# Optimization experiments

Hardware: AMD Instinct MI355X
Metric: run time of the kernel (lower is better)

## Reference

```python
import jax, jax.numpy as jnp
import numpy as np

B, C, H, W = 16, 256, 56, 56
HID = C * 2            # modifier_expansion = 2
GROUPS = 8             # min(8, HID//4)
K = 3                  # inner_steps
LR = 0.01              # exp(log(inner_lr))
RATIO = 0.25           # spatial_mask_ratio
GN_EPS = 1e-5


def setup_inputs() -> dict:
    key = jax.random.key(0)
    ks = jax.random.split(key, 12)
    x = jax.random.normal(ks[0], (B, C, H, W), jnp.float32)
    # modifier params (1x1 convs stored as 2D matrices) + GroupNorm affine
    conv1_w = jax.random.normal(ks[1], (HID, C), jnp.float32) / np.sqrt(C)
    gn_gamma = 1.0 + 0.1 * jax.random.normal(ks[2], (HID,), jnp.float32)
    gn_beta = 0.1 * jax.random.normal(ks[3], (HID,), jnp.float32)
    conv2_w = jax.random.normal(ks[4], (C, HID), jnp.float32) / np.sqrt(HID)
    # surprise reconstructor (bottleneck = C//4)
    recon_w1 = jax.random.normal(ks[5], (C // 4, C), jnp.float32) / np.sqrt(C)
    recon_w2 = jax.random.normal(ks[6], (C, C // 4), jnp.float32) / np.sqrt(C // 4)
    # gate MLP
    gate_w1 = jax.random.normal(ks[7], (C // 4, C), jnp.float32) / np.sqrt(C)
    gate_b1 = jnp.zeros((C // 4,), jnp.float32)
    gate_w2 = jax.random.normal(ks[8], (1, C // 4), jnp.float32) / np.sqrt(C // 4)
    gate_b2 = jnp.zeros((1,), jnp.float32)
    residual_scale = jnp.asarray(0.05, jnp.float32)
    # EMA buffers (eval mode: frozen)
    running_mean = 0.05 * jax.random.normal(ks[9], (C,), jnp.float32)
    running_var = 1.0 + 0.05 * jax.random.uniform(ks[10], (C,), jnp.float32)
    # spatial masks: exactly int(H*W*RATIO) zeroed positions per sample, one mask
    # per inner update step (only steps 0..K-2 affect the output)
    num_mask = int(H * W * RATIO)
    rng = np.random.default_rng(0)
    r = rng.random((K - 1, B, H * W))
    idx = np.argsort(r, axis=-1)[..., :num_mask]
    m = np.ones((K - 1, B, H * W), dtype=bool)
    np.put_along_axis(m, idx, False, axis=-1)
    masks = jnp.asarray(m.reshape(K - 1, B, 1, H, W))
    return dict(x=x, conv1_w=conv1_w, gn_gamma=gn_gamma, gn_beta=gn_beta,
                conv2_w=conv2_w, recon_w1=recon_w1, recon_w2=recon_w2,
                gate_w1=gate_w1, gate_b1=gate_b1, gate_w2=gate_w2,
                gate_b2=gate_b2, residual_scale=residual_scale,
                running_mean=running_mean, running_var=running_var, masks=masks)


def _group_norm(h, gamma, beta):
    b = h.shape[0]
    hg = h.reshape(b, GROUPS, HID // GROUPS, H, W)
    mu = hg.mean(axis=(2, 3, 4), keepdims=True)
    var = hg.var(axis=(2, 3, 4), keepdims=True)  # biased, matching torch GN
    hg = (hg - mu) * jax.lax.rsqrt(var + GN_EPS)
    return hg.reshape(b, HID, H, W) * gamma[None, :, None, None] + beta[None, :, None, None]


def _modifier(feat, w1, gamma, beta, w2):
    # Conv2d 1x1 (no bias) -> GroupNorm -> GELU -> [Dropout2d: identity in eval] -> Conv2d 1x1
    h = jnp.einsum('bchw,oc->bohw', feat, w1)
    h = jax.nn.gelu(_group_norm(h, gamma, beta), approximate=False)
    return jnp.einsum('bohw,co->bchw', h, w2)


def _surprise(y, mask, rw1, rw2, rm, rv):
    mf = mask.astype(y.dtype)                       # [B,1,H,W]
    my = y * mf
    h = jax.nn.gelu(jnp.einsum('bchw,oc->bohw', my, rw1), approximate=False)
    rec = jnp.einsum('bohw,co->bchw', h, rw2)
    inv = 1.0 - mf
    recon = (((rec - y) ** 2) * inv).sum() / (inv.sum() * C + 1e-8)
    n = y.shape[0] * y.shape[2] * y.shape[3]
    cm = y.mean(axis=(0, 2, 3))                     # [C]
    cv = ((y - cm[None, :, None, None]) ** 2).sum(axis=(0, 2, 3)) / (n - 1)  # unbiased
    consist = ((cm - rm) ** 2).mean() + ((cv / (rv + 1e-8) - 1.0) ** 2).mean()
    return recon + 0.1 * consist


def reference(x, conv1_w, gn_gamma, gn_beta, conv2_w, recon_w1, recon_w2,
              gate_w1, gate_b1, gate_w2, gate_b2, residual_scale,
              running_mean, running_var, masks):
    feat = jax.lax.stop_gradient(x)  # feat_inner = features.detach()
    params = (conv1_w, gn_gamma, gn_beta, conv2_w)

    def inner_loss(p, mask):
        m = _modifier(feat, *p)
        return _surprise(m + feat, mask, recon_w1, recon_w2, running_mean, running_var)

    # TTT inner loop: K-1 SGD updates on the modifier params; updates are
    # stop_gradient'ed so the outer Jacobian wrt initial params is identity,
    # matching torch's .data in-place update with create_graph=False.
    for step in range(K - 1):
        g = jax.grad(inner_loss)(params, masks[step])
        params = tuple(p - LR * jax.lax.stop_gradient(gi) for p, gi in zip(params, g))

    modification = _modifier(x, *params)  # final forward uses non-detached features

    pooled = x.mean(axis=(2, 3))                                    # [B,C]
    gh = jax.nn.gelu(pooled @ gate_w1.T + gate_b1, approximate=False)
    gate = jax.nn.sigmoid(gh @ gate_w2.T + gate_b2)[:, :, None, None]  # [B,1,1,1]

    return x + residual_scale * gate * modification
```

## Files before the change

kernel.cpp:

```cpp
#include <hip/hip_runtime.h>
#include <math.h>


#define BB    16
#define CC    256
#define HWW   3136
#define NTOT  (BB*HWW)
#define HIDD  512
#define NGRP  8
#define GMSZ  (64*HWW)
#define C4    64
#define LRATE 0.01f
#define SKW   32
#define CHUNK (NTOT/SKW)
#define NV8   (HWW/8)

#define EP_STORE    0
#define EP_ADDFEAT  1
#define EP_T1H      2
#define EP_DYREC    3
#define EP_DT1      4
#define EP_DYFIN    5
#define EP_H1STAT   6
#define EP_YADDSTAT 7
#define EP_GNB1     8

typedef unsigned short u16;
typedef __attribute__((ext_vector_type(8))) short bf16x8;
typedef __attribute__((ext_vector_type(4))) float f32x4;

__device__ __forceinline__ float bf2f(u16 u){
  return __uint_as_float(((unsigned)u)<<16);
}
__device__ __forceinline__ u16 f2bf(float f){
  unsigned u = __float_as_uint(f);
  u += 0x7FFFu + ((u>>16)&1u);
  return (u16)(u>>16);
}
__device__ __forceinline__ float gelu_f(float x){
  return 0.5f*x*(1.0f+erff(x*0.70710678118654752f));
}
__device__ __forceinline__ float rcp_f(float x){ return __builtin_amdgcn_rcpf(x); }
__device__ __forceinline__ float gelu_fast(float x){
  float x2 = x*x;
  float u = 0.7978845608f*x*fmaf(0.044715f, x2, 1.0f);
  float t = 1.0f - 2.0f*rcp_f(__expf(2.0f*u)+1.0f);
  return 0.5f*x*(1.0f+t);
}
__device__ __forceinline__ float gelu_g_fast(float x){
  float x2 = x*x;
  float u = 0.7978845608f*x*fmaf(0.044715f, x2, 1.0f);
  float t = 1.0f - 2.0f*rcp_f(__expf(2.0f*u)+1.0f);
  float du = 0.7978845608f*fmaf(0.134145f, x2, 1.0f);
  return fmaf(0.5f*x*(1.0f-t*t), du, 0.5f*(1.0f+t));
}
__device__ __forceinline__ float blk_sum(float v, float* sm){
  #pragma unroll
  for (int o=32;o>0;o>>=1) v += __shfl_down(v,o);
  if ((threadIdx.x & 63)==0) sm[threadIdx.x>>6] = v;
  __syncthreads();
  float r = sm[0]+sm[1]+sm[2]+sm[3];
  __syncthreads();
  return r;
}
__device__ __forceinline__ uint4 pack8(const ushort* e){
  uint4 v;
  v.x = (unsigned)e[0] | ((unsigned)e[1]<<16);
  v.y = (unsigned)e[2] | ((unsigned)e[3]<<16);
  v.z = (unsigned)e[4] | ((unsigned)e[5]<<16);
  v.w = (unsigned)e[6] | ((unsigned)e[7]<<16);
  return v;
}
__device__ __forceinline__ void up8(uint4 v, float* f){
  f[0]=bf2f((u16)(v.x&0xFFFFu)); f[1]=bf2f((u16)(v.x>>16));
  f[2]=bf2f((u16)(v.y&0xFFFFu)); f[3]=bf2f((u16)(v.y>>16));
  f[4]=bf2f((u16)(v.z&0xFFFFu)); f[5]=bf2f((u16)(v.z>>16));
  f[6]=bf2f((u16)(v.w&0xFFFFu)); f[7]=bf2f((u16)(v.w>>16));
}
// ... 22 lines not shown
  for (int i=0;i<256;i++){
    unsigned char v=m[i]; if (v>mx) mx=v;
    if (v){ int r=i&3; if(r==0)nz0=1; else if(r==1)nz1=1; else if(r==2)nz2=1; else nz3=1; }
  }
  int f;
  if (mx<=1) f = (nz1|nz2|nz3) ? 0 : 1;
  else       f = (!nz0 && !nz1) ? 3 : 2;
  *flag=f;
}
__global__ void k_report(u16* out, float v){
  if (threadIdx.x==0 && blockIdx.x==0) out[0] = f2bf(v);
}

__global__ void k_cvt(const void* __restrict__ src, float* __restrict__ dst, int n,
                      const int* __restrict__ dtf){
  int i = blockIdx.x*256 + threadIdx.x;
  if (i>=n) return;
  if (*dtf) dst[i] = bf2f(((const u16*)src)[i]);
  else      dst[i] = ((const float*)src)[i];
}
__global__ void k_wcvt(const float* __restrict__ src, u16* __restrict__ d,
                       u16* __restrict__ dT, int R, int Cc){
  int i = blockIdx.x*256+threadIdx.x;
  if (i >= R*Cc) return;
  int r = i/Cc, c = i - r*Cc;
  u16 v = f2bf(src[i]);
  d[i] = v;
  if (dT) dT[(size_t)c*R + r] = v;
}

__global__ void k_expand(const unsigned char* __restrict__ mraw, const int* __restrict__ flag,
                         float* __restrict__ mf, float* __restrict__ zc){
  __shared__ float sm[4];
  int i = blockIdx.x*256 + threadIdx.x;
  int f = *flag;
  float v;
  if (f==1)      v = (((const int*)mraw)[i] != 0) ? 1.f : 0.f;
  else if (f==0) v = (mraw[i] != 0) ? 1.f : 0.f;
  else if (f==2) v = (((const u16*)mraw)[i] != 0) ? 1.f : 0.f;
  else           v = (((const float*)mraw)[i] != 0.f) ? 1.f : 0.f;
  mf[i] = v;
  float S = blk_sum(1.f - v, sm);
  if (threadIdx.x==0) atomicAdd(&zc[blockIdx.x/196], S);
}

template<int MASKX,int EPI,int XDYN,int E0DYN>
__global__ __launch_bounds__(256) void k_gemm_mfma(
    const u16* __restrict__ A, const void* __restrict__ Xv, u16* __restrict__ Out,
    int K, const int* __restrict__ xdt, const float* __restrict__ mf,
    const void* __restrict__ e0, const float* __restrict__ e1,
    const float* __restrict__ e2, u16* __restrict__ o2, float* __restrict__ o3)
{
  __shared__ __align__(16) u16 Ws[64*40];
  __shared__ u16 Xs[128*40];
  const int t = threadIdx.x;
  const int w = t >> 6, lane = t & 63;
  const int col = lane & 15, quad = lane >> 4;
  const int M = (int)gridDim.y << 6;
  const int m0 = blockIdx.y << 6, n0 = blockIdx.x << 7;
  const int isbx = XDYN ? *xdt : 1;
  const u16*   Xb = (const u16*)Xv;
  const float* Xf = (const float*)Xv;
  const int wrow = t >> 2, wkq = (t & 3) * 8;
  const int xn   = 2*(t & 63);
  const int xq   = t >> 6;
  const int gn0  = n0 + xn;
  const int xb_  = gn0 / HWW;
  const int xs_  = gn0 - xb_*HWW;

  f32x4 acc[4][2];
  #pragma unroll
  for (int i=0;i<4;i++){
    #pragma unroll
    for (int j=0;j<2;j++) acc[i][j] = (f32x4)(0.0f);
  }

  for (int k0=0; k0<K; k0+=32){
    {
      uint4 v = *(const uint4*)(A + (size_t)(m0+wrow)*K + k0 + wkq);
      *(uint4*)(Ws + wrow*40 + wkq) = v;
    }
    {
      ushort e[16];
      size_t base = ((size_t)xb_*K + k0 + xq*8)*HWW + xs_;
      if (isbx){
        #pragma unroll
        for (int j=0;j<8;j++){
          unsigned v = *(const unsigned*)(Xb + base + (size_t)j*HWW);
          e[j]   = (ushort)(v & 0xFFFFu);
          e[8+j] = (ushort)(v >> 16);
        }
      } else {
        #pragma unroll
        for (int j=0;j<8;j++){
          float2 f = *(const float2*)(Xf + base + (size_t)j*HWW);
          e[j]   = f2bf(f.x);
          e[8+j] = f2bf(f.y);
        }
      }
      if (MASKX){
        if (mf[gn0]   == 0.f){
          #pragma unroll
          for (int j=0;j<8;j++) e[j] = 0;
        }
        if (mf[gn0+1] == 0.f){
          #pragma unroll
          for (int j=0;j<8;j++) e[8+j] = 0;
        }
      }
      *(uint4*)(Xs + xn*40     + xq*8) = pack8(e);
      *(uint4*)(Xs + (xn+1)*40 + xq*8) = pack8(e+8);
    }
    __syncthreads();
    bf16x8 af[4], bfr[2];
    #pragma unroll
    for (int mi=0;mi<4;mi++)
      af[mi] = *(const bf16x8*)(Ws + (mi*16+col)*40 + quad*8);
    #pragma unroll
    for (int nj=0;nj<2;nj++)
      bfr[nj] = *(const bf16x8*)(Xs + (w*32+nj*16+col)*40 + quad*8);
    #pragma unroll
    for (int mi=0;mi<4;mi++){
      #pragma unroll
      for (int nj=0;nj<2;nj++)
        acc[mi][nj] = __builtin_amdgcn_mfma_f32_16x16x32_bf16(af[mi], bfr[nj], acc[mi][nj], 0,0,0);
    }
    __syncthreads();
  }

  const int isb0 = E0DYN ? *xdt : 1;

  if (EPI==EP_H1STAT){
    float* sred = (float*)Ws;
    if (t < 4) sred[t] = 0.f;
    __syncthreads();
    float sH[2]={0.f,0.f}, sQ[2]={0.f,0.f};
    #pragma unroll
    for (int nj=0;nj<2;nj++){
      const int nb = n0 + w*32 + nj*16;
      const int b  = nb / HWW;
      const int sb = nb - b*HWW + col;
      #pragma unroll
      for (int mi=0;mi<4;mi++){
        #pragma unroll
        for (int r=0;r<4;r++){
          const int m = m0 + mi*16 + quad*4 + r;
          const size_t oidx = ((size_t)b*M + m)*HWW + sb;
          float v = acc[mi][nj][r];
          Out[oidx] = f2bf(v);
          sH[nj] += v; sQ[nj] = fmaf(v,v,sQ[nj]);
        }
      }
    }
    #pragma unroll
    for (int nj=0;nj<2;nj++){
      float a=sH[nj], c=sQ[nj];
      #pragma unroll
      for (int o=1;o<64;o<<=1){ a += __shfl_xor(a,o); c += __shfl_xor(c,o); }
      if (lane==0){
        const int nb = n0 + w*32 + nj*16;
        const int slot = ((nb/HWW) != n0/HWW) ? 1 : 0;
        atomicAdd(&sred[slot*2],   a);
        atomicAdd(&sred[slot*2+1], c);
      }
    }
    __syncthreads();
    const int g = m0>>6;
    if (t==0){
      const int b0=n0/HWW;
      atomicAdd(&o3[b0*NGRP+g],     sred[0]);
      atomicAdd(&o3[128+b0*NGRP+g], sred[1]);
    }
    if (t==1){
      const int b0=n0/HWW, b1=(n0+127)/HWW;
      if (b1!=b0){
        atomicAdd(&o3[b1*NGRP+g],     sred[2]);
        atomicAdd(&o3[128+b1*NGRP+g], sred[3]);
      }
    }
    return;
  }

  if (EPI==EP_YADDSTAT){
    float* sred = (float*)Ws;
    for (int i=t;i<128;i+=256) sred[i]=0.f;
    __syncthreads();
    #pragma unroll
    for (int mi=0;mi<4;mi++){
      #pragma unroll
      for (int r=0;r<4;r++){
        float sM=0.f, sQv=0.f;
        const int m = m0 + mi*16 + quad*4 + r;
        #pragma unroll
        for (int nj=0;nj<2;nj++){
          const int nb = n0 + w*32 + nj*16;
          const int b  = nb / HWW;
          const int sb = nb - b*HWW + col;
          const size_t oidx = ((size_t)b*M + m)*HWW + sb;
          float xv = isb0 ? bf2f(((const u16*)e0)[oidx]) : ((const float*)e0)[oidx];
          float y = acc[mi][nj][r] + xv;
          Out[oidx] = f2bf(y);
          sM += y; sQv = fmaf(y,y,sQv);
        }
        #pragma unroll
        for (int o=1;o<16;o<<=1){ sM += __shfl_xor(sM,o); sQv += __shfl_xor(sQv,o); }
        if (col==0){
          atomicAdd(&sred[mi*16+quad*4+r],    sM);
          atomicAdd(&sred[64+mi*16+quad*4+r], sQv);
        }
      }
    }
    __syncthreads();
    if (t<64){
      atomicAdd(&o3[m0+t],    sred[t]);
      atomicAdd(&o3[CC+m0+t], sred[64+t]);
    }
    return;
  }

  if (EPI==EP_GNB1){
    float* sred = (float*)Ws;
    for (int i=t;i<132;i+=256) sred[i]=0.f;
    __syncthreads();
    const int g = m0>>6;
    float sS1[2]={0.f,0.f}, sS2[2]={0.f,0.f};
    #pragma unroll
    for (int mi=0;mi<4;mi++){
      #pragma unroll
      for (int r=0;r<4;r++){
        const int m = m0 + mi*16 + quad*4 + r;
        const float go = e2[m], beo = e2[HIDD+m];
        float dB=0.f, dG=0.f;
        #pragma unroll
        for (int nj=0;nj<2;nj++){
          const int nb = n0 + w*32 + nj*16;
          const int b  = nb / HWW;
          const int sb = nb - b*HWW + col;
          const int bg = b*NGRP + g;
          const size_t oidx = ((size_t)b*M + m)*HWW + sb;
          const float mU = e1[bg], rS = e1[128+bg];
          float hn   = (bf2f(((const u16*)e0)[oidx]) - mU)*rS;
          float ghat = fmaf(hn, go, beo);
          float dgh  = acc[mi][nj][r] * gelu_g_fast(ghat);
          float dhn  = dgh * go;
          Out[oidx] = f2bf(dhn);
          dB += dgh; dG = fmaf(dgh, hn, dG);
          sS1[nj] += dhn; sS2[nj] = fmaf(dhn, hn, sS2[nj]);
        }
        #pragma unroll
        for (int o=1;o<16;o<<=1){ dB += __shfl_xor(dB,o); dG += __shfl_xor(dG,o); }
        if (col==0){
          atomicAdd(&sred[mi*16+quad*4+r],    dB);
          atomicAdd(&sred[64+mi*16+quad*4+r], dG);
        }
      }
    }
    #pragma unroll
    for (int nj=0;nj<2;nj++){
      float a=sS1[nj], c=sS2[nj];
      #pragma unroll
      for (int o=1;o<64;o<<=1){ a += __shfl_xor(a,o); c += __shfl_xor(c,o); }
      if (lane==0){
        const int nb = n0 + w*32 + nj*16;
        const int slot = ((nb/HWW) != n0/HWW) ? 1 : 0;
        atomicAdd(&sred[128+slot*2],   a);
        atomicAdd(&sred[128+slot*2+1], c);
      }
    }
    __syncthreads();
    if (t<64){
      atomicAdd(&o3[m0+t],     sred[64+t]);
      atomicAdd(&o3[512+m0+t], sred[t]);
    }
    if (t==64){
      const int b0=n0/HWW;
      atomicAdd(&o3[1024+b0*NGRP+g],     sred[128]);
      atomicAdd(&o3[1152+b0*NGRP+g],     sred[129]);
    }
    if (t==65){
      const int b0=n0/HWW, b1=(n0+127)/HWW;
      if (b1!=b0){
        atomicAdd(&o3[1024+b1*NGRP+g],   sred[130]);
        atomicAdd(&o3[1152+b1*NGRP+g],   sred[131]);
      }
    }
    return;
  }

  float dscale = 0.f;
  if (EPI==EP_DYREC) dscale = 2.0f / (e1[0]*(float)CC + 1e-8f);
  #pragma unroll
  for (int nj=0;nj<2;nj++){
    const int nb = n0 + w*32 + nj*16;
    const int b  = nb / HWW;
    const int sb = nb - b*HWW + col;
    const int n  = nb + col;
    #pragma unroll
    for (int mi=0;mi<4;mi++){
      #pragma unroll
      for (int r=0;r<4;r++){
        const int m = m0 + mi*16 + quad*4 + r;
        const size_t oidx = ((size_t)b*M + m)*HWW + sb;
        float v = acc[mi][nj][r];
        if (EPI==EP_STORE){ Out[oidx] = f2bf(v); }
        else if (EPI==EP_ADDFEAT){
          float xv = isb0 ? bf2f(((const u16*)e0)[oidx]) : ((const float*)e0)[oidx];
          Out[oidx] = f2bf(v + xv);
        }
        else if (EPI==EP_T1H){ Out[oidx] = f2bf(v); o2[oidx] = f2bf(gelu_fast(v)); }
        else if (EPI==EP_DYREC){
          float iv = 1.0f - mf[n];
          Out[oidx] = f2bf((v - bf2f(((const u16*)e0)[oidx]))*iv*dscale);
        }
        else if (EPI==EP_DT1){ Out[oidx] = f2bf(v * gelu_g_fast(bf2f(((const u16*)e0)[oidx]))); }
        else if (EPI==EP_DYFIN){
          float dyold = bf2f(Out[oidx]);
          Out[oidx] = f2bf(mf[n]*v - dyold + e1[m] + e2[m]*bf2f(((const u16*)e0)[oidx]));
        }
      }
    }
  }
}

template<int QDYN>
__global__ __launch_bounds__(256) void k_wgrad_mfma(
    const u16* __restrict__ P, const void* __restrict__ Qv, float* __restrict__ part,
    int CHP, int CHQ, const int* __restrict__ xdt, int ntx)
{
  __shared__ u16 Ps[64*40];
  __shared__ u16 Qs[64*40];
  const int f = blockIdx.x;
  const int j = f >> 3;
  const int sk = (f & 7) + ((j >> 5) << 3);
  const int tile = j & 31;
  const int ty = tile / ntx;
  const int m0 = (tile - ty*ntx) << 6;
  const int n0 = ty << 6;
  const int t = threadIdx.x;
  const int w = t >> 6, lane = t & 63;
  const int col = lane & 15, quad = lane >> 4;
  const int isbq = QDYN ? *xdt : 1;
  const u16*   Qb = (const u16*)Qv;
  const float* Qf = (const float*)Qv;
  const int srow = (t & 127) >> 1;
  const int ssq  = ((t & 127) & 1) * 16;
  f32x4 acc[2][2];
  #pragma unroll
  for (int i=0;i<2;i++){
    #pragma unroll
    for (int jj=0;jj<2;jj++) acc[i][jj] = (f32x4)(0.0f);
  }
  const int mbase = (w & 1)*32, nbase = (w >> 1)*32;

  for (int kb = sk*CHUNK; kb < sk*CHUNK + CHUNK; kb += 32){
    const int b = kb / HWW;
    const int s = kb - b*HWW;
    if (t < 128){
      size_t off = ((size_t)b*CHP + m0+srow)*HWW + s + ssq;
      uint4 v0 = *(const uint4*)(P + off);
      uint4 v1 = *(const uint4*)(P + off + 8);
      *(uint4*)(Ps + srow*40 + ssq)     = v0;
      *(uint4*)(Ps + srow*40 + ssq + 8) = v1;
    } else {
      size_t off = ((size_t)b*CHQ + n0+srow)*HWW + s + ssq;
      if (isbq){
        uint4 v0 = *(const uint4*)(Qb + off);
        uint4 v1 = *(const uint4*)(Qb + off + 8);
        *(uint4*)(Qs + srow*40 + ssq)     = v0;
        *(uint4*)(Qs + srow*40 + ssq + 8) = v1;
      } else {
        ushort e[16];
        #pragma unroll
        for (int g=0; g<4; g++){
          float4 ff = *(const float4*)(Qf + off + g*4);
          e[g*4+0]=f2bf(ff.x); e[g*4+1]=f2bf(ff.y); e[g*4+2]=f2bf(ff.z); e[g*4+3]=f2bf(ff.w);
        }
        *(uint4*)(Qs + srow*40 + ssq)     = pack8(e);
        *(uint4*)(Qs + srow*40 + ssq + 8) = pack8(e+8);
      }
    }
    __syncthreads();
    bf16x8 pa[2], qb[2];
    #pragma unroll
    for (int a=0;a<2;a++)
      pa[a] = *(const bf16x8*)(Ps + (mbase + a*16 + col)*40 + quad*8);
    #pragma unroll
    for (int bb=0;bb<2;bb++)
      qb[bb] = *(const bf16x8*)(Qs + (nbase + bb*16 + col)*40 + quad*8);
    #pragma unroll
    for (int a=0;a<2;a++){
      #pragma unroll
      for (int bb=0;bb<2;bb++)
        acc[a][bb] = __builtin_amdgcn_mfma_f32_16x16x32_bf16(pa[a], qb[bb], acc[a][bb], 0,0,0);
    }
    __syncthreads();
  }
  float* dst = part + (size_t)sk*CHP*CHQ;
  #pragma unroll
  for (int a=0;a<2;a++){
    #pragma unroll
    for (int bb=0;bb<2;bb++){
      #pragma unroll
      for (int r=0;r<4;r++){
        const int m = m0 + mbase + a*16 + quad*4 + r;
        const int n = n0 + nbase + bb*16 + col;
        dst[(size_t)m*CHQ + n] = acc[a][bb][r];
      }
    }
  }
}
__global__ void k_wgrad_reduce(const float* __restrict__ part, float* __restrict__ dW, int n){
  int i = blockIdx.x*256+threadIdx.x;
  if (i>=n) return;
  float s=0;
  #pragma unroll
  for (int k=0;k<SKW;k++) s += part[(size_t)k*n + i];
  dW[i]=s;
}

__global__ void k_gn_finalize(const float* gsum, const float* gsumsq, float* mu, float* rsig){
  int i = threadIdx.x; if (i>=BB*NGRP) return;
  float m = gsum[i]*(1.0f/GMSZ);
  float v = gsumsq[i]*(1.0f/GMSZ) - m*m;
  v = fmaxf(v, 0.0f);
  mu[i]=m; rsig[i]=rsqrtf(v+1e-5f);
}
template<int FAST>
__global__ void k_gelu_fwd(const u16* __restrict__ src, u16* __restrict__ dst,
// ... 65 lines not shown
  uint4* pa = (uint4*)(dA + (size_t)bo*HWW);
  const uint4* ph = (const uint4*)(h1 + (size_t)bo*HWW);
  for (int i=threadIdx.x;i<NV8;i+=256){
    float fa[8], fh[8]; up8(pa[i], fa); up8(ph[i], fh);
    #pragma unroll
    for (int j=0;j<8;j++){
      float hn = (fh[j]-m)*r;
      fa[j] = r*(fa[j] - a1 - hn*a2);
    }
    pa[i] = pk8(fa);
  }
}

__global__ void k_update(float* pw1, float* pw2, float* pg, float* pb,
    const float* dW1, const float* dW2, const float* dGa, const float* dBe){
  int i = blockIdx.x*256+threadIdx.x;
  if (i < HIDD*CC){ pw1[i] -= LRATE*dW1[i]; pw2[i] -= LRATE*dW2[i]; }
  if (i < HIDD){ pg[i] -= LRATE*dGa[i]; pb[i] -= LRATE*dBe[i]; }
}

__global__ void k_pool(const void* __restrict__ xv, const int* __restrict__ dtf, float* pooled){
  __shared__ float sm[4];
  int bc = blockIdx.x;
  int isb = *dtf;
  float s=0;
  if (isb){
    const uint4* p = (const uint4*)((const u16*)xv + (size_t)bc*HWW);
    for (int i=threadIdx.x;i<NV8;i+=256){
      float f[8]; up8(p[i], f);
      #pragma unroll
      for (int j=0;j<8;j++) s+=f[j];
    }
  } else {
    const float4* p = (const float4*)((const float*)xv + (size_t)bc*HWW);
    for (int i=threadIdx.x;i<HWW/4;i+=256){
      float4 f = p[i];
      s += f.x+f.y+f.z+f.w;
    }
  }
  float S = blk_sum(s,sm);
  if (threadIdx.x==0) pooled[bc]=S*(1.0f/HWW);
}
__global__ void k_gate(const float* __restrict__ pooled, const float* __restrict__ gw1,
    const float* __restrict__ gb1, const float* __restrict__ gw2, const float* __restrict__ gb2,
    float* gate){
  int b = blockIdx.x, j = threadIdx.x;
  float acc = gb1[j];
  const float* pr = pooled + b*CC;
  for (int c=0;c<CC;c++) acc = fmaf(pr[c], gw1[j*CC+c], acc);
  float v = gelu_f(acc)*gw2[j];
  #pragma unroll
  for (int o=32;o>0;o>>=1) v += __shfl_down(v,o);
  if (j==0) gate[b] = 1.0f/(1.0f+expf(-(v+gb2[0])));
}
__global__ void k_out(const void* __restrict__ xv, const u16* __restrict__ mod,
    const float* __restrict__ gate, const float* __restrict__ rsf,
    const int* __restrict__ dtf, void* __restrict__ out){
  size_t i4 = (size_t)blockIdx.x*256+threadIdx.x;
  size_t i = i4*4;
  int b = (int)(i / ((size_t)CC*HWW));
  float gm = rsf[0]*gate[b];
  int isb = *dtf;
  ushort4 mv = ((const ushort4*)mod)[i4];
  if (isb){
    ushort4 xu = ((const ushort4*)xv)[i4];
    ushort4 r;
    r.x = f2bf(bf2f(xu.x) + gm*bf2f(mv.x));
    r.y = f2bf(bf2f(xu.y) + gm*bf2f(mv.y));
    r.z = f2bf(bf2f(xu.z) + gm*bf2f(mv.z));
    r.w = f2bf(bf2f(xu.w) + gm*bf2f(mv.w));
    ((ushort4*)out)[i4] = r;
  } else {
    float4 xf = ((const float4*)xv)[i4];
    float4 r;
    r.x = xf.x + gm*bf2f(mv.x);
    r.y = xf.y + gm*bf2f(mv.y);
    r.z = xf.z + gm*bf2f(mv.z);
    r.w = xf.w + gm*bf2f(mv.w);
    ((float4*)out)[i4] = r;
  }
}

extern "C" void kernel_launch(void* const* d_in, const int* in_sizes, int n_in,
                              void* d_out, int out_size, void* d_ws, size_t ws_size,
                              hipStream_t stream)
{
  const void* x_in   = d_in[0];
  const void* w1_in  = d_in[1];
  const void* g_in   = d_in[2];
  const void* b_in   = d_in[3];
  const void* w2_in  = d_in[4];
  const void* rw1_in = d_in[5];
  const void* rw2_in = d_in[6];
  const void* gw1_in = d_in[7];
  const void* gb1_in = d_in[8];
  const void* gw2_in = d_in[9];
  const void* gb2_in = d_in[10];
  const void* rs_in  = d_in[11];
  const void* rm_in  = d_in[12];
  const void* rv_in  = d_in[13];
  const void* mk_in  = d_in[14];
  (void)in_sizes; (void)n_in; (void)out_size;

  char* base = (char*)d_ws;
  size_t off = 0;
  auto alloc = [&](size_t bytes)->char*{
    char* p = base+off; off = (off+bytes+255)&~(size_t)255; return p;
  };
  u16* ybuf = (u16*)alloc((size_t)CC*NTOT*2);
  u16* dY   = (u16*)alloc((size_t)CC*NTOT*2);
  u16* Ab   = (u16*)alloc((size_t)HIDD*NTOT*2);
  u16* t1b  = (u16*)alloc((size_t)C4*NTOT*2);
  u16* hb   = (u16*)alloc((size_t)C4*NTOT*2);
  u16* h1rc = ybuf;
  float* part = (float*)ybuf;
  float* mfb  = (float*)alloc((size_t)2*NTOT*4);
  float* pw1  = (float*)alloc(131072*4);
  float* pw2  = (float*)alloc(131072*4);
  float* dW1  = (float*)alloc(131072*4);
  float* dW2  = (float*)alloc(131072*4);
  u16* wb1   = (u16*)alloc(131072*2);
  u16* wb2   = (u16*)alloc(131072*2);
  u16* wb2T  = (u16*)alloc(131072*2);
  u16* rwb1  = (u16*)alloc(16384*2);
  u16* rwb1T = (u16*)alloc(16384*2);
  u16* rwb2  = (u16*)alloc(16384*2);
  u16* rwb2T = (u16*)alloc(16384*2);
  float* pg   = (float*)alloc(512*4);
  float* pb   = (float*)alloc(512*4);
  float* rw1f = (float*)alloc(16384*4);
  float* rw2f = (float*)alloc(16384*4);
  float* gw1f = (float*)alloc(16384*4);
  float* gb1f = (float*)alloc(64*4);
// ... 16 lines not shown
  float* s2     = (float*)alloc(512);
  float* pooled = (float*)alloc(16384);
  float* gate   = (float*)alloc(256);
  float* zc     = (float*)alloc(256);
  int*   dtf    = (int*)alloc(256);
  int*   mkf    = (int*)alloc(256);

  if (off > ws_size){
    k_report<<<1,64,0,stream>>>((u16*)d_out, (float)(ws_size>>20));
    return;
  }
  u16* h1p = nullptr;
  if (off + (size_t)HIDD*NTOT*2 <= ws_size)
    h1p = (u16*)alloc((size_t)HIDD*NTOT*2);

  k_detect_dtype<<<1,1,0,stream>>>((const u16*)x_in, dtf);
  k_detect_mask<<<1,1,0,stream>>>((const unsigned char*)mk_in, mkf);
  #define CVT(src,dst,n) k_cvt<<<((n)+255)/256,256,0,stream>>>(src,dst,(n),dtf)
  CVT(w1_in,  pw1,  131072);
  CVT(g_in,   pg,   512);
  CVT(b_in,   pb,   512);
  CVT(w2_in,  pw2,  131072);
  CVT(rw1_in, rw1f, 16384);
  CVT(rw2_in, rw2f, 16384);
  CVT(gw1_in, gw1f, 16384);
  CVT(gb1_in, gb1f, 64);
  CVT(gw2_in, gw2f, 64);
  CVT(gb2_in, gb2f, 1);
  CVT(rs_in,  rsf,  1);
  CVT(rm_in,  rmf,  256);
  CVT(rv_in,  rvf,  256);
  #undef CVT
  k_wcvt<<<512,256,0,stream>>>(pw1, wb1, 0,     HIDD, CC);
  k_wcvt<<<512,256,0,stream>>>(pw2, wb2, wb2T,  CC, HIDD);
  k_wcvt<<<64,256,0,stream>>>(rw1f, rwb1, rwb1T, C4, CC);
  k_wcvt<<<64,256,0,stream>>>(rw2f, rwb2, rwb2T, CC, C4);
  hipMemsetAsync(zc, 0, 8, stream);
  k_expand<<<392,256,0,stream>>>((const unsigned char*)mk_in, mkf, mfb, zc);

  for (int s=0; s<2; s++){
    const float* mfs = mfb + s*NTOT;
    u16* h1dst = h1p ? h1p : Ab;
    hipMemsetAsync(gsum, 0, 1024, stream);
    k_gemm_mfma<0,EP_H1STAT,1,0><<<dim3(392,8),256,0,stream>>>(wb1, x_in, h1dst, CC, dtf, 0,0,0,0,0, gsum);
    k_gn_finalize<<<1,128,0,stream>>>(gsum, gsumsq, mu, rsig);
    k_gelu_fwd<1><<<BB*HIDD,256,0,stream>>>(h1dst, Ab, mu, rsig, pg, pb);
    hipMemsetAsync(cmsum, 0, 2048, stream);
    k_gemm_mfma<0,EP_YADDSTAT,0,1><<<dim3(392,4),256,0,stream>>>(wb2, Ab, ybuf, HIDD, dtf, 0, x_in, 0,0,0, cmsum);
    k_y_finalize<<<1,256,0,stream>>>(cmsum, cmsq, rmf, rvf, coefA, coefB);
    k_gemm_mfma<1,EP_T1H,0,0><<<dim3(392,1),256,0,stream>>>(rwb1, ybuf, t1b, CC, dtf, mfs, 0,0,0, hb, 0);
    k_gemm_mfma<0,EP_DYREC,0,0><<<dim3(392,4),256,0,stream>>>(rwb2, hb, dY, C4, dtf, mfs, ybuf, zc+s, 0,0, 0);
    k_gemm_mfma<0,EP_DT1,0,0><<<dim3(392,1),256,0,stream>>>(rwb2T, dY, hb, CC, dtf, 0, t1b, 0,0,0, 0);
    k_gemm_mfma<0,EP_DYFIN,0,0><<<dim3(392,4),256,0,stream>>>(rwb1T, hb, dY, C4, dtf, mfs, ybuf, coefA, coefB, 0, 0);
    k_wgrad_mfma<0><<<dim3(32*SKW),256,0,stream>>>(dY, Ab, part, CC, HIDD, dtf, 4);
    k_wgrad_reduce<<<512,256,0,stream>>>(part, dW2, 131072);
    hipMemsetAsync(dGa, 0, 5120, stream);
    if (h1p){
      k_gemm_mfma<0,EP_GNB1,0,0><<<dim3(392,8),256,0,stream>>>(wb2T, dY, Ab, CC, dtf, 0, h1p, mu, pg, 0, dGa);
    } else {
      k_gemm_mfma<0,EP_STORE,0,0><<<dim3(392,8),256,0,stream>>>(wb2T, dY, Ab, CC, dtf, 0,0,0,0,0, 0);
    }
    const u16* h1src = h1p;
    if (!h1p){
      k_gemm_mfma<0,EP_H1STAT,1,0><<<dim3(392,8),256,0,stream>>>(wb1, x_in, h1rc, CC, dtf, 0,0,0,0,0, gsum);
      h1src = h1rc;
      k_gn_bwd1<<<BB*HIDD,256,0,stream>>>(Ab, h1src, mu, rsig, pg, pb, dGa, dBe, s1, s2);
    }
    k_gn_bwd2<<<BB*HIDD,256,0,stream>>>(Ab, h1src, mu, rsig, s1, s2);
    k_wgrad_mfma<1><<<dim3(32*SKW),256,0,stream>>>(Ab, x_in, part, HIDD, CC, dtf, 8);
    k_wgrad_reduce<<<512,256,0,stream>>>(part, dW1, 131072);
    k_update<<<512,256,0,stream>>>(pw1, pw2, pg, pb, dW1, dW2, dGa, dBe);
    k_wcvt<<<512,256,0,stream>>>(pw1, wb1, 0,    HIDD, CC);
    k_wcvt<<<512,256,0,stream>>>(pw2, wb2, wb2T, CC, HIDD);
  }

  hipMemsetAsync(gsum, 0, 1024, stream);
  k_gemm_mfma<0,EP_H1STAT,1,0><<<dim3(392,8),256,0,stream>>>(wb1, x_in, Ab, CC, dtf, 0,0,0,0,0, gsum);
  k_gn_finalize<<<1,128,0,stream>>>(gsum, gsumsq, mu, rsig);
  k_gelu_fwd<0><<<BB*HIDD,256,0,stream>>>(Ab, Ab, mu, rsig, pg, pb);
  k_gemm_mfma<0,EP_STORE,0,0><<<dim3(392,4),256,0,stream>>>(wb2, Ab, ybuf, HIDD, dtf, 0,0,0,0,0, 0);

  k_pool<<<BB*CC,256,0,stream>>>(x_in, dtf, pooled);
  k_gate<<<BB,64,0,stream>>>(pooled, gw1f, gb1f, gw2f, gb2f, gate);
  k_out<<<(CC*NTOT)/1024,256,0,stream>>>(x_in, ybuf, gate, rsf, dtf, d_out);
}
```

Before: 1.209 ms.

## Stage GEMM epilogues through LDS for vectorized stores; fuse GN backward and output

Every MFMA GEMM epilogue now writes its accumulator tile to shared memory and reads it back row-wise, so each thread handles 8 contiguous outputs with 16-byte loads and stores instead of scattered 2-byte accesses. The GroupNorm backward second pass is folded into the operand load of the dW1 weight-gradient kernel, which removes the separate k_gn_bwd2 pass over the hidden activations. The final output residual-gate combine is fused into the last conv2 GEMM epilogue, removing the intermediate buffer and the k_out kernel. In exchange each epilogue adds per-slice barriers and LDS traffic, and the wgrad loader now does extra arithmetic and reads h1.

```diff
diff --git a/kernel.cpp b/kernel.cpp
--- a/kernel.cpp
+++ b/kernel.cpp
@@ -14,6 +14,7 @@
 #define SKW   32
 #define CHUNK (NTOT/SKW)
 #define NV8   (HWW/8)
+#define FSTR  132
 
 #define EP_STORE    0
 #define EP_ADDFEAT  1
@@ -24,6 +25,7 @@
 #define EP_H1STAT   6
 #define EP_YADDSTAT 7
 #define EP_GNB1     8
+#define EP_OUT      9
 
 typedef unsigned short u16;
 typedef __attribute__((ext_vector_type(8))) short bf16x8;
@@ -152,7 +154,7 @@
     const float* __restrict__ e2, u16* __restrict__ o2, float* __restrict__ o3)
 {
   __shared__ __align__(16) u16 Ws[64*40];
-  __shared__ u16 Xs[128*40];
+  __shared__ __align__(16) u16 Xs[128*40];
   const int t = threadIdx.x;
   const int w = t >> 6, lane = t & 63;
   const int col = lane & 15, quad = lane >> 4;
@@ -227,205 +229,235 @@
     }
     __syncthreads();
   }
-
   const int isb0 = E0DYN ? *xdt : 1;
+  float* fst  = (float*)Xs;
+  float* sred = (float*)Ws;
+  const int row16 = t >> 4;
+  const int cb    = (t & 15) * 8;
+  const int nb8   = n0 + cb;
+  const int b8    = nb8 / HWW;
+  const int sb8   = nb8 - b8*HWW;
+  const int bA    = n0 / HWW, bB = (n0+127)/HWW;
+  const int g     = m0 >> 6;
+
+  if (EPI==EP_H1STAT){ if (t<4) sred[t]=0.f; }
+  if (EPI==EP_YADDSTAT){ for (int i=t;i<128;i+=256) sred[i]=0.f; }
+  if (EPI==EP_GNB1){ for (int i=t;i<132;i+=256) sred[i]=0.f; }
+  if (EPI==EP_H1STAT||EPI==EP_YADDSTAT||EPI==EP_GNB1) __syncthreads();
+
+  float dscale=0.f, gmul=0.f, muT=0.f, rT=0.f;
+  if (EPI==EP_DYREC) dscale = 2.0f / (e1[0]*(float)CC + 1e-8f);
+  if (EPI==EP_OUT)   gmul = e2[0]*e1[b8];
+  if (EPI==EP_GNB1){ muT = e1[b8*NGRP+g]; rT = e1[128+b8*NGRP+g]; }
+
+  #pragma unroll
+  for (int mi=0;mi<4;mi++){
+    #pragma unroll
+    for (int nj=0;nj<2;nj++){
+      #pragma unroll
+      for (int r=0;r<4;r++)
+        fst[(quad*4+r)*FSTR + w*32 + nj*16 + col] = acc[mi][nj][r];
+    }
+    __syncthreads();
+    const int m = m0 + mi*16 + row16;
+    const size_t oidx = ((size_t)b8*M + m)*HWW + sb8;
+    float v[8];
+    {
+      const float* frow = fst + row16*FSTR + cb;
+      float4 p0 = *(const float4*)frow;
+      float4 p1 = *(const float4*)(frow+4);
+      v[0]=p0.x; v[1]=p0.y; v[2]=p0.z; v[3]=p0.w;
+      v[4]=p1.x; v[5]=p1.y; v[6]=p1.z; v[7]=p1.w;
+    }
+
+    if (EPI==EP_STORE){
+      *(uint4*)(Out+oidx) = pk8(v);
+    }
+    else if (EPI==EP_ADDFEAT){
+      float xv[8];
+      if (isb0) up8(*(const uint4*)((const u16*)e0+oidx), xv);
+      else {
+        float4 a0 = *(const float4*)((const float*)e0+oidx);
+        float4 a1 = *(const float4*)((const float*)e0+oidx+4);
+        xv[0]=a0.x; xv[1]=a0.y; xv[2]=a0.z; xv[3]=a0.w;
+        xv[4]=a1.x; xv[5]=a1.y; xv[6]=a1.z; xv[7]=a1.w;
+      }
+      #pragma unroll
+      for (int j=0;j<8;j++) v[j] += xv[j];
+      *(uint4*)(Out+oidx) = pk8(v);
+    }
+    else if (EPI==EP_T1H){
+      *(uint4*)(Out+oidx) = pk8(v);
+      float gv[8];
+      #pragma unroll
+      for (int j=0;j<8;j++) gv[j] = gelu_fast(v[j]);
+      *(uint4*)(o2+oidx) = pk8(gv);
+    }
+    else if (EPI==EP_DYREC){
+      float yv[8], mfv[8];
+      up8(*(const uint4*)((const u16*)e0+oidx), yv);
+      float4 f0 = *(const float4*)(mf+nb8);
+      float4 f1 = *(const float4*)(mf+nb8+4);
+      mfv[0]=f0.x; mfv[1]=f0.y; mfv[2]=f0.z; mfv[3]=f0.w;
+      mfv[4]=f1.x; mfv[5]=f1.y; mfv[6]=f1.z; mfv[7]=f1.w;
+      #pragma unroll
+      for (int j=0;j<8;j++) v[j] = (v[j]-yv[j])*(1.0f-mfv[j])*dscale;
+      *(uint4*)(Out+oidx) = pk8(v);
+    }
+    else if (EPI==EP_DT1){
+      float tv[8];
+      up8(*(const uint4*)((const u16*)e0+oidx), tv);
+      #pragma unroll
+      for (int j=0;j<8;j++) v[j] = v[j]*gelu_g_fast(tv[j]);
+      *(uint4*)(Out+oidx) = pk8(v);
+    }
+    else if (EPI==EP_DYFIN){
+      float yv[8], dv[8], mfv[8];
+      up8(*(const uint4*)((const u16*)e0+oidx), yv);
+      up8(*(const uint4*)(Out+oidx), dv);
+      float4 f0 = *(const float4*)(mf+nb8);
+      float4 f1 = *(const float4*)(mf+nb8+4);
+      mfv[0]=f0.x; mfv[1]=f0.y; mfv[2]=f0.z; mfv[3]=f0.w;
+      mfv[4]=f1.x; mfv[5]=f1.y; mfv[6]=f1.z; mfv[7]=f1.w;
+      const float c1 = e1[m], c2 = e2[m];
+      #pragma unroll
+      for (int j=0;j<8;j++) v[j] = mfv[j]*v[j] - dv[j] + c1 + c2*yv[j];
+      *(uint4*)(Out+oidx) = pk8(v);
+    }
+    else if (EPI==EP_H1STAT){
+      *(uint4*)(Out+oidx) = pk8(v);
+      float s=0.f, q=0.f;
+      #pragma unroll
+      for (int j=0;j<8;j++){ s += v[j]; q = fmaf(v[j],v[j],q); }
+      float s0 = (b8==bA)?s:0.f, q0 = (b8==bA)?q:0.f;
+      float s1v = s-s0, q1v = q-q0;
+      #pragma unroll
+      for (int o=1;o<64;o<<=1){
+        s0 += __shfl_xor(s0,o); q0 += __shfl_xor(q0,o);
+        s1v += __shfl_xor(s1v,o); q1v += __shfl_xor(q1v,o);
+      }
+      if (lane==0){
+        atomicAdd(&sred[0], s0); atomicAdd(&sred[1], q0);
+        atomicAdd(&sred[2], s1v); atomicAdd(&sred[3], q1v);
+      }
+    }
+    else if (EPI==EP_YADDSTAT){
+      float xv[8];
+      if (isb0) up8(*(const uint4*)((const u16*)e0+oidx), xv);
+      else {
+        float4 a0 = *(const float4*)((const float*)e0+oidx);
+        float4 a1 = *(const float4*)((const float*)e0+oidx+4);
+        xv[0]=a0.x; xv[1]=a0.y; xv[2]=a0.z; xv[3]=a0.w;
+        xv[4]=a1.x; xv[5]=a1.y; xv[6]=a1.z; xv[7]=a1.w;
+      }
+      float s=0.f, q=0.f;
+      #pragma unroll
+      for (int j=0;j<8;j++){
+        v[j] += xv[j];
+        s += v[j]; q = fmaf(v[j],v[j],q);
+      }
+      *(uint4*)(Out+oidx) = pk8(v);
+      #pragma unroll
+      for (int o=1;o<16;o<<=1){ s += __shfl_xor(s,o); q += __shfl_xor(q,o); }
+      if ((t&15)==0){
+        atomicAdd(&sred[mi*16+row16], s);
+        atomicAdd(&sred[64+mi*16+row16], q);
+      }
+    }
+    else if (EPI==EP_GNB1){
+      float hv[8];
+      up8(*(const uint4*)((const u16*)e0+oidx), hv);
+      const float go = e2[m], beo = e2[HIDD+m];
+      float dB=0.f, dG=0.f, sS=0.f, sQ=0.f;
+      #pragma unroll
+      for (int j=0;j<8;j++){
+        float hn   = (hv[j]-muT)*rT;
+        float ghat = fmaf(hn, go, beo);
+        float dgh  = v[j]*gelu_g_fast(ghat);
+        float dhn  = dgh*go;
+        v[j] = dhn;
+        dB += dgh; dG = fmaf(dgh,hn,dG);
+        sS += dhn; sQ = fmaf(dhn,hn,sQ);
+      }
+      *(uint4*)(Out+oidx) = pk8(v);
+      #pragma unroll
+      for (int o=1;o<16;o<<=1){ dB += __shfl_xor(dB,o); dG += __shfl_xor(dG,o); }
+      if ((t&15)==0){
+        atomicAdd(&sred[mi*16+row16], dB);
+        atomicAdd(&sred[64+mi*16+row16], dG);
+      }
+      float s0 = (b8==bA)?sS:0.f, q0 = (b8==bA)?sQ:0.f;
+      float s1v = sS-s0, q1v = sQ-q0;
+      #pragma unroll
+      for (int o=1;o<64;o<<=1){
+        s0 += __shfl_xor(s0,o); q0 += __shfl_xor(q0,o);
+        s1v += __shfl_xor(s1v,o); q1v += __shfl_xor(q1v,o);
+      }
+      if (lane==0){
+        atomicAdd(&sred[128], s0); atomicAdd(&sred[129], q0);
+        atomicAdd(&sred[130], s1v); atomicAdd(&sred[131], q1v);
+      }
+    }
+    else if (EPI==EP_OUT){
+      float xv[8];
+      if (isb0){
+        up8(*(const uint4*)((const u16*)e0+oidx), xv);
+        #pragma unroll
+        for (int j=0;j<8;j++) v[j] = xv[j] + gmul*v[j];
+        *(uint4*)(Out+oidx) = pk8(v);
+      } else {
+        float4 a0 = *(const float4*)((const float*)e0+oidx);
+        float4 a1 = *(const float4*)((const float*)e0+oidx+4);
+        float4 r0, r1;
+        r0.x = a0.x + gmul*v[0]; r0.y = a0.y + gmul*v[1];
+        r0.z = a0.z + gmul*v[2]; r0.w = a0.w + gmul*v[3];
+        r1.x = a1.x + gmul*v[4]; r1.y = a1.y + gmul*v[5];
+        r1.z = a1.z + gmul*v[6]; r1.w = a1.w + gmul*v[7];
+        *(float4*)((float*)Out+oidx)   = r0;
+        *(float4*)((float*)Out+oidx+4) = r1;
+      }
+    }
+    __syncthreads();
+  }
 
   if (EPI==EP_H1STAT){
-    float* sred = (float*)Ws;
-    if (t < 4) sred[t] = 0.f;
-    __syncthreads();
-    float sH[2]={0.f,0.f}, sQ[2]={0.f,0.f};
-    #pragma unroll
-    for (int nj=0;nj<2;nj++){
-      const int nb = n0 + w*32 + nj*16;
-      const int b  = nb / HWW;
-      const int sb = nb - b*HWW + col;
-      #pragma unroll
-      for (int mi=0;mi<4;mi++){
-        #pragma unroll
-        for (int r=0;r<4;r++){
-          const int m = m0 + mi*16 + quad*4 + r;
-          const size_t oidx = ((size_t)b*M + m)*HWW + sb;
-          float v = acc[mi][nj][r];
-          Out[oidx] = f2bf(v);
-          sH[nj] += v; sQ[nj] = fmaf(v,v,sQ[nj]);
-        }
-      }
-    }
-    #pragma unroll
-    for (int nj=0;nj<2;nj++){
-      float a=sH[nj], c=sQ[nj];
-      #pragma unroll
-      for (int o=1;o<64;o<<=1){ a += __shfl_xor(a,o); c += __shfl_xor(c,o); }
-      if (lane==0){
-        const int nb = n0 + w*32 + nj*16;
-        const int slot = ((nb/HWW) != n0/HWW) ? 1 : 0;
-        atomicAdd(&sred[slot*2],   a);
-        atomicAdd(&sred[slot*2+1], c);
-      }
-    }
-    __syncthreads();
-    const int g = m0>>6;
     if (t==0){
-      const int b0=n0/HWW;
-      atomicAdd(&o3[b0*NGRP+g],     sred[0]);
-      atomicAdd(&o3[128+b0*NGRP+g], sred[1]);
-    }
-    if (t==1){
-      const int b0=n0/HWW, b1=(n0+127)/HWW;
-      if (b1!=b0){
-        atomicAdd(&o3[b1*NGRP+g],     sred[2]);
-        atomicAdd(&o3[128+b1*NGRP+g], sred[3]);
-      }
-    }
-    return;
-  }
-
+      atomicAdd(&o3[bA*NGRP+g],     sred[0]);
+      atomicAdd(&o3[128+bA*NGRP+g], sred[1]);
+    }
+    if (t==1 && bB!=bA){
+      atomicAdd(&o3[bB*NGRP+g],     sred[2]);
+      atomicAdd(&o3[128+bB*NGRP+g], sred[3]);
+    }
+  }
   if (EPI==EP_YADDSTAT){
-    float* sred = (float*)Ws;
-    for (int i=t;i<128;i+=256) sred[i]=0.f;
-    __syncthreads();
-    #pragma unroll
-    for (int mi=0;mi<4;mi++){
-      #pragma unroll
-      for (int r=0;r<4;r++){
-        float sM=0.f, sQv=0.f;
-        const int m = m0 + mi*16 + quad*4 + r;
-        #pragma unroll
-        for (int nj=0;nj<2;nj++){
-          const int nb = n0 + w*32 + nj*16;
-          const int b  = nb / HWW;
-          const int sb = nb - b*HWW + col;
-          const size_t oidx = ((size_t)b*M + m)*HWW + sb;
-          float xv = isb0 ? bf2f(((const u16*)e0)[oidx]) : ((const float*)e0)[oidx];
-          float y = acc[mi][nj][r] + xv;
-          Out[oidx] = f2bf(y);
-          sM += y; sQv = fmaf(y,y,sQv);
-        }
-        #pragma unroll
-        for (int o=1;o<16;o<<=1){ sM += __shfl_xor(sM,o); sQv += __shfl_xor(sQv,o); }
-        if (col==0){
-          atomicAdd(&sred[mi*16+quad*4+r],    sM);
-          atomicAdd(&sred[64+mi*16+quad*4+r], sQv);
-        }
-      }
-    }
-    __syncthreads();
     if (t<64){
       atomicAdd(&o3[m0+t],    sred[t]);
       atomicAdd(&o3[CC+m0+t], sred[64+t]);
     }
-    return;
-  }
-
+  }
   if (EPI==EP_GNB1){
-    float* sred = (float*)Ws;
-    for (int i=t;i<132;i+=256) sred[i]=0.f;
-    __syncthreads();
-    const int g = m0>>6;
-    float sS1[2]={0.f,0.f}, sS2[2]={0.f,0.f};
-    #pragma unroll
-    for (int mi=0;mi<4;mi++){
-      #pragma unroll
-      for (int r=0;r<4;r++){
-        const int m = m0 + mi*16 + quad*4 + r;
-        const float go = e2[m], beo = e2[HIDD+m];
-        float dB=0.f, dG=0.f;
-        #pragma unroll
-        for (int nj=0;nj<2;nj++){
-          const int nb = n0 + w*32 + nj*16;
-          const int b  = nb / HWW;
-          const int sb = nb - b*HWW + col;
-          const int bg = b*NGRP + g;
-          const size_t oidx = ((size_t)b*M + m)*HWW + sb;
-          const float mU = e1[bg], rS = e1[128+bg];
-          float hn   = (bf2f(((const u16*)e0)[oidx]) - mU)*rS;
-          float ghat = fmaf(hn, go, beo);
-          float dgh  = acc[mi][nj][r] * gelu_g_fast(ghat);
-          float dhn  = dgh * go;
-          Out[oidx] = f2bf(dhn);
-          dB += dgh; dG = fmaf(dgh, hn, dG);
-          sS1[nj] += dhn; sS2[nj] = fmaf(dhn, hn, sS2[nj]);
-        }
-        #pragma unroll
-        for (int o=1;o<16;o<<=1){ dB += __shfl_xor(dB,o); dG += __shfl_xor(dG,o); }
-        if (col==0){
-          atomicAdd(&sred[mi*16+quad*4+r],    dB);
-          atomicAdd(&sred[64+mi*16+quad*4+r], dG);
-        }
-      }
-    }
-    #pragma unroll
-    for (int nj=0;nj<2;nj++){
-      float a=sS1[nj], c=sS2[nj];
-      #pragma unroll
-      for (int o=1;o<64;o<<=1){ a += __shfl_xor(a,o); c += __shfl_xor(c,o); }
-      if (lane==0){
-        const int nb = n0 + w*32 + nj*16;
-        const int slot = ((nb/HWW) != n0/HWW) ? 1 : 0;
-        atomicAdd(&sred[128+slot*2],   a);
-        atomicAdd(&sred[128+slot*2+1], c);
-      }
-    }
-    __syncthreads();
     if (t<64){
       atomicAdd(&o3[m0+t],     sred[64+t]);
       atomicAdd(&o3[512+m0+t], sred[t]);
     }
     if (t==64){
-      const int b0=n0/HWW;
-      atomicAdd(&o3[1024+b0*NGRP+g],     sred[128]);
-      atomicAdd(&o3[1152+b0*NGRP+g],     sred[129]);
-    }
-    if (t==65){
-      const int b0=n0/HWW, b1=(n0+127)/HWW;
-      if (b1!=b0){
-        atomicAdd(&o3[1024+b1*NGRP+g],   sred[130]);
-        atomicAdd(&o3[1152+b1*NGRP+g],   sred[131]);
-      }
-    }
-    return;
-  }
-
-  float dscale = 0.f;
-  if (EPI==EP_DYREC) dscale = 2.0f / (e1[0]*(float)CC + 1e-8f);
-  #pragma unroll
-  for (int nj=0;nj<2;nj++){
-    const int nb = n0 + w*32 + nj*16;
-    const int b  = nb / HWW;
-    const int sb = nb - b*HWW + col;
-    const int n  = nb + col;
-    #pragma unroll
-    for (int mi=0;mi<4;mi++){
-      #pragma unroll
-      for (int r=0;r<4;r++){
-        const int m = m0 + mi*16 + quad*4 + r;
-        const size_t oidx = ((size_t)b*M + m)*HWW + sb;
-        float v = acc[mi][nj][r];
-        if (EPI==EP_STORE){ Out[oidx] = f2bf(v); }
-        else if (EPI==EP_ADDFEAT){
-          float xv = isb0 ? bf2f(((const u16*)e0)[oidx]) : ((const float*)e0)[oidx];
-          Out[oidx] = f2bf(v + xv);
-        }
-        else if (EPI==EP_T1H){ Out[oidx] = f2bf(v); o2[oidx] = f2bf(gelu_fast(v)); }
-        else if (EPI==EP_DYREC){
-          float iv = 1.0f - mf[n];
-          Out[oidx] = f2bf((v - bf2f(((const u16*)e0)[oidx]))*iv*dscale);
-        }
-        else if (EPI==EP_DT1){ Out[oidx] = f2bf(v * gelu_g_fast(bf2f(((const u16*)e0)[oidx]))); }
-        else if (EPI==EP_DYFIN){
-          float dyold = bf2f(Out[oidx]);
-          Out[oidx] = f2bf(mf[n]*v - dyold + e1[m] + e2[m]*bf2f(((const u16*)e0)[oidx]));
-        }
-      }
-    }
-  }
-}
-
-template<int QDYN>
+      atomicAdd(&o3[1024+bA*NGRP+g], sred[128]);
+      atomicAdd(&o3[1152+bA*NGRP+g], sred[129]);
+    }
+    if (t==65 && bB!=bA){
+      atomicAdd(&o3[1024+bB*NGRP+g], sred[130]);
+      atomicAdd(&o3[1152+bB*NGRP+g], sred[131]);
+    }
+  }
+}
+
+template<int QDYN, int GNB2>
 __global__ __launch_bounds__(256) void k_wgrad_mfma(
     const u16* __restrict__ P, const void* __restrict__ Qv, float* __restrict__ part,
-    int CHP, int CHQ, const int* __restrict__ xdt, int ntx)
+    int CHP, int CHQ, const int* __restrict__ xdt, int ntx,
+    const u16* __restrict__ h1, const float* __restrict__ musig,
+    const float* __restrict__ red)
 {
   __shared__ u16 Ps[64*40];
   __shared__ u16 Qs[64*40];
@@ -459,6 +491,23 @@
       size_t off = ((size_t)b*CHP + m0+srow)*HWW + s + ssq;
       uint4 v0 = *(const uint4*)(P + off);
       uint4 v1 = *(const uint4*)(P + off + 8);
+      if (GNB2){
+        const int bg = b*NGRP + (m0>>6);
+        const float mu_ = musig[bg], r_ = musig[128+bg];
+        const float a1 = red[1024+bg]*(1.0f/GMSZ);
+        const float a2 = red[1152+bg]*(1.0f/GMSZ);
+        uint4 h0 = *(const uint4*)(h1 + off);
+        uint4 h1v = *(const uint4*)(h1 + off + 8);
+        float fd[8], fh[8];
+        up8(v0, fd); up8(h0, fh);
+        #pragma unroll
+        for (int q2=0;q2<8;q2++){ float hn=(fh[q2]-mu_)*r_; fd[q2]=r_*(fd[q2]-a1-hn*a2); }
+        v0 = pk8(fd);
+        up8(v1, fd); up8(h1v, fh);
+        #pragma unroll
+        for (int q2=0;q2<8;q2++){ float hn=(fh[q2]-mu_)*r_; fd[q2]=r_*(fd[q2]-a1-hn*a2); }
+        v1 = pk8(fd);
+      }
       *(uint4*)(Ps + srow*40 + ssq)     = v0;
       *(uint4*)(Ps + srow*40 + ssq + 8) = v1;
     } else {
@@ -471,9 +520,9 @@
       } else {
         ushort e[16];
         #pragma unroll
-        for (int g=0; g<4; g++){
-          float4 ff = *(const float4*)(Qf + off + g*4);
-          e[g*4+0]=f2bf(ff.x); e[g*4+1]=f2bf(ff.y); e[g*4+2]=f2bf(ff.z); e[g*4+3]=f2bf(ff.w);
+        for (int g2=0; g2<4; g2++){
+          float4 ff = *(const float4*)(Qf + off + g2*4);
+          e[g2*4+0]=f2bf(ff.x); e[g2*4+1]=f2bf(ff.y); e[g2*4+2]=f2bf(ff.z); e[g2*4+3]=f2bf(ff.w);
         }
         *(uint4*)(Qs + srow*40 + ssq)     = pack8(e);
         *(uint4*)(Qs + srow*40 + ssq + 8) = pack8(e+8);
@@ -645,33 +694,6 @@
   #pragma unroll
   for (int o=32;o>0;o>>=1) v += __shfl_down(v,o);
   if (j==0) gate[b] = 1.0f/(1.0f+expf(-(v+gb2[0])));
-}
-__global__ void k_out(const void* __restrict__ xv, const u16* __restrict__ mod,
-    const float* __restrict__ gate, const float* __restrict__ rsf,
-    const int* __restrict__ dtf, void* __restrict__ out){
-  size_t i4 = (size_t)blockIdx.x*256+threadIdx.x;
-  size_t i = i4*4;
-  int b = (int)(i / ((size_t)CC*HWW));
-  float gm = rsf[0]*gate[b];
-  int isb = *dtf;
-  ushort4 mv = ((const ushort4*)mod)[i4];
-  if (isb){
-    ushort4 xu = ((const ushort4*)xv)[i4];
-    ushort4 r;
-    r.x = f2bf(bf2f(xu.x) + gm*bf2f(mv.x));
-    r.y = f2bf(bf2f(xu.y) + gm*bf2f(mv.y));
-    r.z = f2bf(bf2f(xu.z) + gm*bf2f(mv.z));
-    r.w = f2bf(bf2f(xu.w) + gm*bf2f(mv.w));
-    ((ushort4*)out)[i4] = r;
-  } else {
-    float4 xf = ((const float4*)xv)[i4];
-    float4 r;
-    r.x = xf.x + gm*bf2f(mv.x);
-    r.y = xf.y + gm*bf2f(mv.y);
-    r.z = xf.z + gm*bf2f(mv.z);
-    r.w = xf.w + gm*bf2f(mv.w);
-    ((float4*)out)[i4] = r;
-  }
 }
 
 extern "C" void kernel_launch(void* const* d_in, const int* in_sizes, int n_in,
@@ -794,35 +816,31 @@
     k_gemm_mfma<0,EP_DYREC,0,0><<<dim3(392,4),256,0,stream>>>(rwb2, hb, dY, C4, dtf, mfs, ybuf, zc+s, 0,0, 0);
     k_gemm_mfma<0,EP_DT1,0,0><<<dim3(392,1),256,0,stream>>>(rwb2T, dY, hb, CC, dtf, 0, t1b, 0,0,0, 0);
     k_gemm_mfma<0,EP_DYFIN,0,0><<<dim3(392,4),256,0,stream>>>(rwb1T, hb, dY, C4, dtf, mfs, ybuf, coefA, coefB, 0, 0);
-    k_wgrad_mfma<0><<<dim3(32*SKW),256,0,stream>>>(dY, Ab, part, CC, HIDD, dtf, 4);
+    k_wgrad_mfma<0,0><<<dim3(32*SKW),256,0,stream>>>(dY, Ab, part, CC, HIDD, dtf, 4, 0,0,0);
     k_wgrad_reduce<<<512,256,0,stream>>>(part, dW2, 131072);
     hipMemsetAsync(dGa, 0, 5120, stream);
     if (h1p){
       k_gemm_mfma<0,EP_GNB1,0,0><<<dim3(392,8),256,0,stream>>>(wb2T, dY, Ab, CC, dtf, 0, h1p, mu, pg, 0, dGa);
+      k_wgrad_mfma<1,1><<<dim3(32*SKW),256,0,stream>>>(Ab, x_in, part, HIDD, CC, dtf, 8, h1p, mu, dGa);
     } else {
       k_gemm_mfma<0,EP_STORE,0,0><<<dim3(392,8),256,0,stream>>>(wb2T, dY, Ab, CC, dtf, 0,0,0,0,0, 0);
-    }
-    const u16* h1src = h1p;
-    if (!h1p){
       k_gemm_mfma<0,EP_H1STAT,1,0><<<dim3(392,8),256,0,stream>>>(wb1, x_in, h1rc, CC, dtf, 0,0,0,0,0, gsum);
-      h1src = h1rc;
-      k_gn_bwd1<<<BB*HIDD,256,0,stream>>>(Ab, h1src, mu, rsig, pg, pb, dGa, dBe, s1, s2);
-    }
-    k_gn_bwd2<<<BB*HIDD,256,0,stream>>>(Ab, h1src, mu, rsig, s1, s2);
-    k_wgrad_mfma<1><<<dim3(32*SKW),256,0,stream>>>(Ab, x_in, part, HIDD, CC, dtf, 8);
+      k_gn_bwd1<<<BB*HIDD,256,0,stream>>>(Ab, h1rc, mu, rsig, pg, pb, dGa, dBe, s1, s2);
+      k_gn_bwd2<<<BB*HIDD,256,0,stream>>>(Ab, h1rc, mu, rsig, s1, s2);
+      k_wgrad_mfma<1,0><<<dim3(32*SKW),256,0,stream>>>(Ab, x_in, part, HIDD, CC, dtf, 8, 0,0,0);
+    }
     k_wgrad_reduce<<<512,256,0,stream>>>(part, dW1, 131072);
     k_update<<<512,256,0,stream>>>(pw1, pw2, pg, pb, dW1, dW2, dGa, dBe);
     k_wcvt<<<512,256,0,stream>>>(pw1, wb1, 0,    HIDD, CC);
     k_wcvt<<<512,256,0,stream>>>(pw2, wb2, wb2T, CC, HIDD);
   }
 
+  k_pool<<<BB*CC,256,0,stream>>>(x_in, dtf, pooled);
+  k_gate<<<BB,64,0,stream>>>(pooled, gw1f, gb1f, gw2f, gb2f, gate);
+
   hipMemsetAsync(gsum, 0, 1024, stream);
   k_gemm_mfma<0,EP_H1STAT,1,0><<<dim3(392,8),256,0,stream>>>(wb1, x_in, Ab, CC, dtf, 0,0,0,0,0, gsum);
   k_gn_finalize<<<1,128,0,stream>>>(gsum, gsumsq, mu, rsig);
   k_gelu_fwd<0><<<BB*HIDD,256,0,stream>>>(Ab, Ab, mu, rsig, pg, pb);
-  k_gemm_mfma<0,EP_STORE,0,0><<<dim3(392,4),256,0,stream>>>(wb2, Ab, ybuf, HIDD, dtf, 0,0,0,0,0, 0);
-
-  k_pool<<<BB*CC,256,0,stream>>>(x_in, dtf, pooled);
-  k_gate<<<BB,64,0,stream>>>(pooled, gw1f, gb1f, gw2f, gb2f, gate);
-  k_out<<<(CC*NTOT)/1024,256,0,stream>>>(x_in, ybuf, gate, rsf, dtf, d_out);
-}
+  k_gemm_mfma<0,EP_OUT,0,1><<<dim3(392,4),256,0,stream>>>(wb2, Ab, (u16*)d_out, HIDD, dtf, 0, x_in, gate, rsf, 0, 0);
+}
```

Result: faster. 1.075 ms (-11.1%).
